# Performance work log

Hardware: AMD Instinct MI355X
Metric: run time of the kernel (lower is better)

## Reference

```python
import jax, jax.numpy as jnp
import numpy as np

T1 = float(np.tan(np.pi / 8))
T3 = float(np.tan(3 * np.pi / 8))

# directional angle ranges in dir_filters() order: hor('0'), dg1('pi4'), ver('pi2'), dg2('3pi4')
DIR_RANGES = [(-T1, T1), (T1, T3), (T3, -T3), (-T3, -T1)]


def _dir_masks():
    # For each direction: (mask[0], mask[2]) 3x3 neighbor-pick kernels (mask[1] is identity = x itself)
    hor = ([[0, 1, 0], [0, 0, 0], [0, 0, 0]], [[0, 0, 0], [0, 0, 0], [0, 1, 0]])
    dg1 = ([[1, 0, 0], [0, 0, 0], [0, 0, 0]], [[0, 0, 0], [0, 0, 0], [0, 0, 1]])
    ver = ([[0, 0, 0], [1, 0, 0], [0, 0, 0]], [[0, 0, 0], [0, 0, 1], [0, 0, 0]])
    dg2 = ([[0, 0, 1], [0, 0, 0], [0, 0, 0]], [[0, 0, 0], [0, 0, 0], [1, 0, 0]])
    m = np.array([hor, dg1, ver, dg2], dtype=np.float32)  # [4,2,3,3]
    return m.reshape(8, 1, 3, 3)


def _gauss_kernel(size=5, sigma=1.0):
    ax = np.arange(size, dtype=np.float32) - (size - 1) / 2
    g = np.exp(-((ax / sigma) ** 2) / 2)
    k = np.outer(g, g)
    return (k / k.sum()).astype(np.float32)


def setup_inputs() -> dict:
    key = jax.random.key(0)
    x = jax.random.uniform(key, (16, 3, 512, 512), dtype=jnp.float32)
    return {"x": x, "low_threshold": 1}


def reference(x, low_threshold):
    B, C, H, W = x.shape
    dn = ('NCHW', 'OIHW', 'NCHW')
    # ---- Gaussian smoothing (gauss=True path), depthwise 5x5, zero pad 2 ----
    gk = jnp.asarray(_gauss_kernel(), x.dtype)
    gw = jnp.tile(gk[None, None], (C, 1, 1, 1))  # [3,1,5,5]
    x = jax.lax.conv_general_dilated(x, gw, (1, 1), [(2, 2), (2, 2)],
                                     feature_group_count=C, dimension_numbers=dn)
    # ---- Sobel gradients (normalized kernels, replicate padding) ----
    kx = jnp.asarray(np.array([[-1, 0, 1], [-2, 0, 2], [-1, 0, 1]], np.float32) / 8.0, x.dtype)
    ky = kx.T  # [[-1,-2,-1],[0,0,0],[1,2,1]]/8
    sob = jnp.stack([kx, ky])[:, None]  # [2,1,3,3]
    xp = jnp.pad(x, ((0, 0), (0, 0), (1, 1), (1, 1)), mode='edge').reshape(B * C, 1, H + 2, W + 2)
    g = jax.lax.conv_general_dilated(xp, sob, (1, 1), 'VALID', dimension_numbers=dn)
    g = g.reshape(B, C, 2, H, W)
    gx_all, gy_all = g[:, :, 0], g[:, :, 1]  # [B,3,H,W]
    mag_all = jnp.sqrt(gx_all * gx_all + gy_all * gy_all + 1e-9)
    idx = jnp.argmax(mag_all, axis=1)  # channel with max magnitude per pixel [B,H,W]
    gx = jnp.take_along_axis(gx_all, idx[:, None], axis=1)[:, 0]
    gy = jnp.take_along_axis(gy_all, idx[:, None], axis=1)[:, 0]
    magnitude = jnp.sqrt(gx * gx + gy * gy + 1e-9)  # [B,H,W]
    gy_safe = jnp.where(gy == 0.0, jnp.asarray(1e-9, x.dtype), gy)
    angle = jnp.clip(gx / gy_safe, -10.0, 10.0)
    # ---- Directional non-maximum suppression ----
    mk = jnp.asarray(_dir_masks(), x.dtype)  # [8,1,3,3]
    neigh = jax.lax.conv_general_dilated(magnitude[:, None], mk, (1, 1), [(1, 1), (1, 1)],
                                         dimension_numbers=dn)  # [B,8,H,W]
    suppressed = jnp.zeros_like(magnitude)
    for d, (lo, hi) in enumerate(DIR_RANGES):
        mx = jnp.maximum(jnp.maximum(neigh[:, 2 * d], neigh[:, 2 * d + 1]), magnitude)
        nms = (mx == magnitude).astype(x.dtype) * magnitude
        if lo < hi:
            dirm = ((lo <= angle) & (angle < hi)).astype(x.dtype)
        else:
            dirm = ((lo <= angle) | (angle < hi)).astype(x.dtype)
        suppressed = suppressed + nms * dirm
    # ---- Threshold + sigmoid ----
    t = jnp.asarray(low_threshold, x.dtype)
    out = jax.nn.sigmoid(jnp.where(suppressed >= t, suppressed, jnp.asarray(1e-9, x.dtype)))
    return out
```

## Files before the change

### kernel.cpp

```cpp
#include <hip/hip_runtime.h>
#include <math.h>


typedef float v2f __attribute__((ext_vector_type(2)));

#define HDIM 512
#define WDIM 512
#define PLANE (HDIM * WDIM)
#define SH   8
#define NSTR (HDIM / SH)
#define NGRP 5
#define GW   112

__device__ __forceinline__ float shfl1(float v, int src) {
    return __shfl(v, src, 64);
}

template<bool RE, bool CE>
__device__ __forceinline__ void run(
    const float* __restrict__ xb0, float t, float* __restrict__ out,
    int b, int R0, int c0, int lane)
{
    const bool colok = !CE || ((unsigned)c0 < (unsigned)WDIM);

    const float w0 = 0.05448868454964294f;
    const float w1 = 0.24420134200323332f;
    const float w2 = 0.4026199468942475f;
    const float T1c = 0.41421356237309503f;
    const float T3c = 2.414213562373095f;

    auto ld2 = [&](int c, int ri) -> v2f {
        if ((CE && !colok) || (RE && (unsigned)ri >= (unsigned)HDIM)) {
            v2f z = {0.f, 0.f};
            return z;
        }
        return *(const v2f*)(xb0 + c * PLANE + ri * WDIM + c0);
    };
    auto hb2 = [&](v2f v) -> v2f {
        v2f L, R;
        L.x = shfl1(v.x, lane - 1); L.y = shfl1(v.y, lane - 1);
        R.x = shfl1(v.x, lane + 1); R.y = shfl1(v.y, lane + 1);
        v2f p = {L.y, v.x};
        v2f q = {v.y, R.x};
        return w0 * (L + R) + w1 * (p + q) + w2 * v;
    };
    auto dirof = [&](float gx, float gy) -> int {
        const float gys = (gy == 0.f) ? 1e-9f : gy;
        const float sg  = (gys > 0.f) ? 1.f : -1.f;
        const float gxs = gx * sg;
        const float gya = fabsf(gys);
        const float a3 = T3c * gya, a1 = T1c * gya;
        return (gxs >= a3 || gxs < -a3) ? 2
             : (gxs >= a1) ? 1
             : (gxs >= -a1) ? 0 : 3;
    };

    v2f xw0[3], xw1[3], xw2[3], xw3[3];
    v2f xn1[3], xn2[3];
    v2f blA[3], blB[3], blC[3];
    v2f mg0 = {0.f, 0.f}, mg1 = {0.f, 0.f}, mg2 = {0.f, 0.f};
    int d1x = 0, d1y = 0, d2x = 0, d2y = 0;

    #pragma unroll
    for (int c = 0; c < 3; ++c) {
        v2f t0 = ld2(c, R0 - 4), t1 = ld2(c, R0 - 3), t2 = ld2(c, R0 - 2);
        v2f t3 = ld2(c, R0 - 1), t4 = ld2(c, R0),     t5 = ld2(c, R0 + 1);
        v2f t6 = ld2(c, R0 + 2);
        v2f vA = w0 * (t0 + t4) + w1 * (t1 + t3) + w2 * t2;
        v2f vB = w0 * (t1 + t5) + w1 * (t2 + t4) + w2 * t3;
        v2f vC = w0 * (t2 + t6) + w1 * (t3 + t5) + w2 * t4;
        blA[c] = hb2(vA);
        blB[c] = hb2(vB);
        blC[c] = hb2(vC);
        xw0[c] = t3; xw1[c] = t4; xw2[c] = t5; xw3[c] = t6;
        xn1[c] = ld2(c, R0 + 3);
        xn2[c] = ld2(c, R0 + 4);
    }

    auto nms_store = [&](int row) {
        float m0l = shfl1(mg0.y, lane - 1), m0r = shfl1(mg0.x, lane + 1);
        float m1l = shfl1(mg1.y, lane - 1), m1r = shfl1(mg1.x, lane + 1);
        float m2l = shfl1(mg2.y, lane - 1), m2r = shfl1(mg2.x, lane + 1);
        float n1x = (d1x == 0) ? mg0.x : (d1x == 1) ? m0l
                  : (d1x == 2) ? m1l   : mg0.y;
        float n2x = (d1x == 0) ? mg2.x : (d1x == 1) ? mg2.y
                  : (d1x == 2) ? mg1.y : m2l;
        float n1y = (d1y == 0) ? mg0.y : (d1y == 1) ? mg0.x
                  : (d1y == 2) ? mg1.x : m0r;
        float n2y = (d1y == 0) ? mg2.y : (d1y == 1) ? m2r
                  : (d1y == 2) ? m1r   : mg2.x;
        float sx = (mg1.x >= n1x && mg1.x >= n2x) ? mg1.x : 0.f;
        float sy = (mg1.y >= n1y && mg1.y >= n2y) ? mg1.y : 0.f;
        float vx = (sx >= t) ? sx : 1e-9f;
        float vy = (sy >= t) ? sy : 1e-9f;
        v2f o;
        o.x = __builtin_amdgcn_rcpf(1.f + __expf(-vx));
        o.y = __builtin_amdgcn_rcpf(1.f + __expf(-vy));
        bool doit = (lane >= 4 && lane < 60);
        if (CE) doit = doit && colok;
        if (doit)
            *(v2f*)&out[((size_t)b * HDIM + row) * WDIM + c0] = o;
    };

    for (int m = R0 - 1; m <= R0 + SH; ++m) {
        v2f xn[3];
        #pragma unroll
        for (int c = 0; c < 3; ++c) {
            xn[c]  = xn1[c];
            xn1[c] = xn2[c];
            xn2[c] = ld2(c, m + 6);
        }

        if (m >= R0 + 2) nms_store(m - 2);

        v2f best = {-1.f, -1.f}, bgx = {0.f, 0.f}, bgy = {0.f, 0.f};
        #pragma unroll
        for (int c = 0; c < 3; ++c) {
            v2f bm = blA[c], b0 = blB[c], bp = blC[c];
            if (RE) {
                if (m == 0)        bm = b0;
                if (m == HDIM - 1) bp = b0;
            }
            v2f tt = bm + 2.f * b0 + bp;
            v2f uu = bp - bm;
            float tly = shfl1(tt.y, lane - 1), trx = shfl1(tt.x, lane + 1);
            float uly = shfl1(uu.y, lane - 1), urx = shfl1(uu.x, lane + 1);
            if (CE) {
                if (c0 == 0)            { tly = tt.x; uly = uu.x; }
                if (c0 + 1 == WDIM - 1) { trx = tt.y; urx = uu.y; }
            }
            v2f gA = {tt.y, trx}, gB = {tly, tt.x};
            v2f gxv = 0.125f * (gA - gB);
            v2f hA = {uly, uu.x}, hB = {uu.y, urx};
            v2f gyv = 0.125f * (hA + 2.f * uu + hB);
            v2f m2v = gxv * gxv + gyv * gyv;
            if (m2v.x > best.x) { best.x = m2v.x; bgx.x = gxv.x; bgy.x = gyv.x; }
            if (m2v.y > best.y) { best.y = m2v.y; bgx.y = gxv.y; bgy.y = gyv.y; }
        }

        #pragma unroll
        for (int c = 0; c < 3; ++c) {
            v2f vb2 = w0 * (xw0[c] + xn[c]) + w1 * (xw1[c] + xw3[c])
                    + w2 * xw2[c];
            v2f blD = hb2(vb2);
            blA[c] = blB[c]; blB[c] = blC[c]; blC[c] = blD;
            xw0[c] = xw1[c]; xw1[c] = xw2[c]; xw2[c] = xw3[c]; xw3[c] = xn[c];
        }

        v2f mag2;
        mag2.x = __builtin_amdgcn_sqrtf(best.x + 1e-9f);
        mag2.y = __builtin_amdgcn_sqrtf(best.y + 1e-9f);
        if (RE && (unsigned)m >= (unsigned)HDIM) { mag2.x = 0.f; mag2.y = 0.f; }
        if (CE && !colok)                        { mag2.x = 0.f; mag2.y = 0.f; }
        const int dnx = dirof(bgx.x, bgy.x);
        const int dny = dirof(bgx.y, bgy.y);
        mg0 = mg1; mg1 = mg2; mg2 = mag2;
        d1x = d2x; d1y = d2y; d2x = dnx; d2y = dny;
    }
    nms_store(R0 + SH - 1);
}

__global__ __launch_bounds__(256) void canny_pipe(
    const float* __restrict__ x, const int* __restrict__ lt,
    float* __restrict__ out)
{
    const int lane = threadIdx.x & 63;
    const int wid  = __builtin_amdgcn_readfirstlane(
                         blockIdx.x * 4 + (threadIdx.x >> 6));
    const int b    = wid / (NGRP * NSTR);
    const int rem  = wid - b * (NGRP * NSTR);
    const int g    = rem >> 6;
    const int s    = rem & (NSTR - 1);
    const int R0   = s * SH;
    const int c0   = g * GW + 2 * lane - 8;
    const float t  = (float)lt[0];
    const float* xb0 = x + (size_t)(b * 3) * PLANE;

    const bool re = (s == 0) || (s == NSTR - 1);
    const bool ce = (g == 0) || (g == NGRP - 1);
    if (!re && !ce)      run<false, false>(xb0, t, out, b, R0, c0, lane);
    else if (!re)        run<false, true >(xb0, t, out, b, R0, c0, lane);
    else if (!ce)        run<true,  false>(xb0, t, out, b, R0, c0, lane);
    else                 run<true,  true >(xb0, t, out, b, R0, c0, lane);
}

extern "C" void kernel_launch(void* const* d_in, const int* in_sizes, int n_in,
                              void* d_out, int out_size, void* d_ws, size_t ws_size,
                              hipStream_t stream) {
    const float* x  = (const float*)d_in[0];
    const int*   lt = (const int*)d_in[1];
    float* out = (float*)d_out;
    const int nblocks = (16 * NGRP * NSTR) / 4;
    canny_pipe<<<nblocks, dim3(256), 0, stream>>>(x, lt, out);
}
```

Before: 111.3 us.

## Software-pipeline cross-lane shuffles one row ahead in the Canny row loop

Restructures the per-row loop so the shuffle-dependent parts of each stage are issued one iteration ahead: horizontal blur inputs, Sobel row partials, and the magnitude neighbour values. These results are carried in registers into the next iteration, so their latency can overlap with independent arithmetic instead of stalling the dependency chain. It also unrolls the loop by two and prefetches one more row. The cost is more live registers, which may reduce occupancy, plus a small amount of extra work at the prologue and tail.

```diff
diff --git a/kernel.cpp b/kernel.cpp
--- a/kernel.cpp
+++ b/kernel.cpp
@@ -57,38 +57,49 @@
 
     v2f xw0[3], xw1[3], xw2[3], xw3[3];
     v2f xn1[3], xn2[3];
-    v2f blA[3], blB[3], blC[3];
+    v2f vbO[3];
+    float vbLx[3], vbLy[3], vbRx[3], vbRy[3];
+    v2f blB[3], blC[3];
+    v2f ttO[3], uuO[3];
+    float ttL[3], ttR[3], uuL[3], uuR[3];
     v2f mg0 = {0.f, 0.f}, mg1 = {0.f, 0.f}, mg2 = {0.f, 0.f};
+    float s0l = 0.f, s0r = 0.f, s1l = 0.f, s1r = 0.f, s2l = 0.f, s2r = 0.f;
     int d1x = 0, d1y = 0, d2x = 0, d2y = 0;
 
     #pragma unroll
     for (int c = 0; c < 3; ++c) {
-        v2f t0 = ld2(c, R0 - 4), t1 = ld2(c, R0 - 3), t2 = ld2(c, R0 - 2);
-        v2f t3 = ld2(c, R0 - 1), t4 = ld2(c, R0),     t5 = ld2(c, R0 + 1);
-        v2f t6 = ld2(c, R0 + 2);
-        v2f vA = w0 * (t0 + t4) + w1 * (t1 + t3) + w2 * t2;
-        v2f vB = w0 * (t1 + t5) + w1 * (t2 + t4) + w2 * t3;
-        v2f vC = w0 * (t2 + t6) + w1 * (t3 + t5) + w2 * t4;
-        blA[c] = hb2(vA);
+        v2f p0 = ld2(c, R0 - 4), p1 = ld2(c, R0 - 3), p2 = ld2(c, R0 - 2);
+        v2f p3 = ld2(c, R0 - 1), p4 = ld2(c, R0),     p5 = ld2(c, R0 + 1);
+        v2f p6 = ld2(c, R0 + 2), p7 = ld2(c, R0 + 3);
+        v2f vA = w0 * (p0 + p4) + w1 * (p1 + p3) + w2 * p2;
+        v2f vB = w0 * (p1 + p5) + w1 * (p2 + p4) + w2 * p3;
+        v2f vC = w0 * (p2 + p6) + w1 * (p3 + p5) + w2 * p4;
+        v2f vD = w0 * (p3 + p7) + w1 * (p4 + p6) + w2 * p5;
+        v2f blA = hb2(vA);
         blB[c] = hb2(vB);
         blC[c] = hb2(vC);
-        xw0[c] = t3; xw1[c] = t4; xw2[c] = t5; xw3[c] = t6;
-        xn1[c] = ld2(c, R0 + 3);
-        xn2[c] = ld2(c, R0 + 4);
+        vbO[c] = vD;
+        vbLx[c] = shfl1(vD.x, lane - 1); vbLy[c] = shfl1(vD.y, lane - 1);
+        vbRx[c] = shfl1(vD.x, lane + 1); vbRy[c] = shfl1(vD.y, lane + 1);
+        xw0[c] = p4; xw1[c] = p5; xw2[c] = p6; xw3[c] = p7;
+        xn1[c] = ld2(c, R0 + 4);
+        xn2[c] = ld2(c, R0 + 5);
+        v2f bm = blA, b0 = blB[c], bp = blC[c];
+        ttO[c] = bm + 2.f * b0 + bp;
+        uuO[c] = bp - bm;
+        ttL[c] = shfl1(ttO[c].y, lane - 1); ttR[c] = shfl1(ttO[c].x, lane + 1);
+        uuL[c] = shfl1(uuO[c].y, lane - 1); uuR[c] = shfl1(uuO[c].x, lane + 1);
     }
 
     auto nms_store = [&](int row) {
-        float m0l = shfl1(mg0.y, lane - 1), m0r = shfl1(mg0.x, lane + 1);
-        float m1l = shfl1(mg1.y, lane - 1), m1r = shfl1(mg1.x, lane + 1);
-        float m2l = shfl1(mg2.y, lane - 1), m2r = shfl1(mg2.x, lane + 1);
-        float n1x = (d1x == 0) ? mg0.x : (d1x == 1) ? m0l
-                  : (d1x == 2) ? m1l   : mg0.y;
+        float n1x = (d1x == 0) ? mg0.x : (d1x == 1) ? s0l
+                  : (d1x == 2) ? s1l   : mg0.y;
         float n2x = (d1x == 0) ? mg2.x : (d1x == 1) ? mg2.y
-                  : (d1x == 2) ? mg1.y : m2l;
+                  : (d1x == 2) ? mg1.y : s2l;
         float n1y = (d1y == 0) ? mg0.y : (d1y == 1) ? mg0.x
-                  : (d1y == 2) ? mg1.x : m0r;
-        float n2y = (d1y == 0) ? mg2.y : (d1y == 1) ? m2r
-                  : (d1y == 2) ? m1r   : mg2.x;
+                  : (d1y == 2) ? mg1.x : s0r;
+        float n2y = (d1y == 0) ? mg2.y : (d1y == 1) ? s2r
+                  : (d1y == 2) ? s1r   : mg2.x;
         float sx = (mg1.x >= n1x && mg1.x >= n2x) ? mg1.x : 0.f;
         float sy = (mg1.y >= n1y && mg1.y >= n2y) ? mg1.y : 0.f;
         float vx = (sx >= t) ? sx : 1e-9f;
@@ -102,65 +113,87 @@
             *(v2f*)&out[((size_t)b * HDIM + row) * WDIM + c0] = o;
     };
 
+    #pragma unroll 2
     for (int m = R0 - 1; m <= R0 + SH; ++m) {
-        v2f xn[3];
+        v2f xn[3], blD[3];
         #pragma unroll
         for (int c = 0; c < 3; ++c) {
             xn[c]  = xn1[c];
             xn1[c] = xn2[c];
-            xn2[c] = ld2(c, m + 6);
+            xn2[c] = ld2(c, m + 7);
         }
 
         if (m >= R0 + 2) nms_store(m - 2);
 
+        #pragma unroll
+        for (int c = 0; c < 3; ++c) {
+            v2f L = {vbLx[c], vbLy[c]}, Rr = {vbRx[c], vbRy[c]};
+            v2f p = {L.y, vbO[c].x};
+            v2f q = {vbO[c].y, Rr.x};
+            blD[c] = w0 * (L + Rr) + w1 * (p + q) + w2 * vbO[c];
+        }
+
         v2f best = {-1.f, -1.f}, bgx = {0.f, 0.f}, bgy = {0.f, 0.f};
         #pragma unroll
         for (int c = 0; c < 3; ++c) {
-            v2f bm = blA[c], b0 = blB[c], bp = blC[c];
-            if (RE) {
-                if (m == 0)        bm = b0;
-                if (m == HDIM - 1) bp = b0;
+            float tly = ttL[c], trx = ttR[c], uly = uuL[c], urx = uuR[c];
+            if (CE) {
+                if (c0 == 0)            { tly = ttO[c].x; uly = uuO[c].x; }
+                if (c0 + 1 == WDIM - 1) { trx = ttO[c].y; urx = uuO[c].y; }
             }
-            v2f tt = bm + 2.f * b0 + bp;
-            v2f uu = bp - bm;
-            float tly = shfl1(tt.y, lane - 1), trx = shfl1(tt.x, lane + 1);
-            float uly = shfl1(uu.y, lane - 1), urx = shfl1(uu.x, lane + 1);
-            if (CE) {
-                if (c0 == 0)            { tly = tt.x; uly = uu.x; }
-                if (c0 + 1 == WDIM - 1) { trx = tt.y; urx = uu.y; }
-            }
-            v2f gA = {tt.y, trx}, gB = {tly, tt.x};
+            v2f gA = {ttO[c].y, trx}, gB = {tly, ttO[c].x};
             v2f gxv = 0.125f * (gA - gB);
-            v2f hA = {uly, uu.x}, hB = {uu.y, urx};
-            v2f gyv = 0.125f * (hA + 2.f * uu + hB);
+            v2f hA = {uly, uuO[c].x}, hB = {uuO[c].y, urx};
+            v2f gyv = 0.125f * (hA + 2.f * uuO[c] + hB);
             v2f m2v = gxv * gxv + gyv * gyv;
             if (m2v.x > best.x) { best.x = m2v.x; bgx.x = gxv.x; bgy.x = gyv.x; }
             if (m2v.y > best.y) { best.y = m2v.y; bgx.y = gxv.y; bgy.y = gyv.y; }
         }
-
-        #pragma unroll
-        for (int c = 0; c < 3; ++c) {
-            v2f vb2 = w0 * (xw0[c] + xn[c]) + w1 * (xw1[c] + xw3[c])
-                    + w2 * xw2[c];
-            v2f blD = hb2(vb2);
-            blA[c] = blB[c]; blB[c] = blC[c]; blC[c] = blD;
-            xw0[c] = xw1[c]; xw1[c] = xw2[c]; xw2[c] = xw3[c]; xw3[c] = xn[c];
-        }
-
-        v2f mag2;
-        mag2.x = __builtin_amdgcn_sqrtf(best.x + 1e-9f);
-        mag2.y = __builtin_amdgcn_sqrtf(best.y + 1e-9f);
-        if (RE && (unsigned)m >= (unsigned)HDIM) { mag2.x = 0.f; mag2.y = 0.f; }
-        if (CE && !colok)                        { mag2.x = 0.f; mag2.y = 0.f; }
+        v2f mag2v;
+        mag2v.x = __builtin_amdgcn_sqrtf(best.x + 1e-9f);
+        mag2v.y = __builtin_amdgcn_sqrtf(best.y + 1e-9f);
+        if (RE && (unsigned)m >= (unsigned)HDIM) { mag2v.x = 0.f; mag2v.y = 0.f; }
+        if (CE && !colok)                        { mag2v.x = 0.f; mag2v.y = 0.f; }
         const int dnx = dirof(bgx.x, bgy.x);
         const int dny = dirof(bgx.y, bgy.y);
-        mg0 = mg1; mg1 = mg2; mg2 = mag2;
+
+        #pragma unroll
+        for (int c = 0; c < 3; ++c) {
+            v2f bm = blB[c], b0 = blC[c], bp = blD[c];
+            if (RE) {
+                if (m + 1 == 0)        bm = b0;
+                if (m + 1 == HDIM - 1) bp = b0;
+            }
+            ttO[c] = bm + 2.f * b0 + bp;
+            uuO[c] = bp - bm;
+            ttL[c] = shfl1(ttO[c].y, lane - 1); ttR[c] = shfl1(ttO[c].x, lane + 1);
+            uuL[c] = shfl1(uuO[c].y, lane - 1); uuR[c] = shfl1(uuO[c].x, lane + 1);
+        }
+
+        #pragma unroll
+        for (int c = 0; c < 3; ++c) {
+            v2f vbN = w0 * (xw0[c] + xn[c]) + w1 * (xw1[c] + xw3[c])
+                    + w2 * xw2[c];
+            vbO[c] = vbN;
+            vbLx[c] = shfl1(vbN.x, lane - 1); vbLy[c] = shfl1(vbN.y, lane - 1);
+            vbRx[c] = shfl1(vbN.x, lane + 1); vbRy[c] = shfl1(vbN.y, lane + 1);
+            xw0[c] = xw1[c]; xw1[c] = xw2[c]; xw2[c] = xw3[c]; xw3[c] = xn[c];
+        }
+
+        s0l = shfl1(mg1.y, lane - 1);   s0r = shfl1(mg1.x, lane + 1);
+        s1l = shfl1(mg2.y, lane - 1);   s1r = shfl1(mg2.x, lane + 1);
+        s2l = shfl1(mag2v.y, lane - 1); s2r = shfl1(mag2v.x, lane + 1);
+
+        blB[0] = blC[0]; blC[0] = blD[0];
+        blB[1] = blC[1]; blC[1] = blD[1];
+        blB[2] = blC[2]; blC[2] = blD[2];
+        mg0 = mg1; mg1 = mg2; mg2 = mag2v;
         d1x = d2x; d1y = d2y; d2x = dnx; d2y = dny;
     }
     nms_store(R0 + SH - 1);
 }
 
-__global__ __launch_bounds__(256) void canny_pipe(
+__global__ __launch_bounds__(256) void canny_fp(
     const float* __restrict__ x, const int* __restrict__ lt,
     float* __restrict__ out)
 {
@@ -191,5 +224,5 @@
     const int*   lt = (const int*)d_in[1];
     float* out = (float*)d_out;
     const int nblocks = (16 * NGRP * NSTR) / 4;
-    canny_pipe<<<nblocks, dim3(256), 0, stream>>>(x, lt, out);
-}
+    canny_fp<<<nblocks, dim3(256), 0, stream>>>(x, lt, out);
+}
```

New measurement: 110.2 us. No clear change (-1.0%).
